# Kernel tuning notes

Hardware: AMD Instinct MI355X
Metric: run time of the kernel (lower is better)

Reference implementation:

```python
import jax, jax.numpy as jnp
import numpy as np

# model dims
B, L, D, K = 4, 1024, 512, 24      # batch, seq_len, d_model, num_eigh
KU, KY, NL, DT = 3, 2, 4, 512      # ar depth u, ar depth y, num_layers, d_target
EPS = 1e-5


def _hankel_eigh():
    # Hankel matrix Z[i,j] = 2 / ((i+j)^3 - (i+j)), i,j in 1..L; top-K eigenpairs
    idx = np.arange(1, L + 1, dtype=np.float64)
    s = idx[:, None] + idx[None, :]
    Z = 2.0 / (s ** 3 - s)
    vals, vecs = np.linalg.eigh(Z)  # ascending
    return (jnp.asarray(vals[-K:], jnp.float32),       # [K]
            jnp.asarray(vecs[:, -K:], jnp.float32))    # [L, K]


def setup_inputs() -> dict:
    key = jax.random.key(0)
    ks = jax.random.split(key, 12)
    sc = 1.0 / np.sqrt(D)
    eig_vals, eig_vecs = _hankel_eigh()
    return {
        "inputs": jax.random.normal(ks[0], (B, L, D), jnp.float32),
        "emb_w": jax.random.normal(ks[1], (D, D), jnp.float32) * sc,
        "emb_b": jnp.zeros((D,), jnp.float32),
        "ln_scale": jnp.ones((NL, D), jnp.float32),
        "ln_bias": jnp.zeros((NL, D), jnp.float32),
        "m_y": jax.random.normal(ks[2], (NL, D, KY, D), jnp.float32) * 0.02,
        "m_u": jax.random.normal(ks[3], (NL, D, D, KU), jnp.float32) * sc,
        "m_phi": jax.random.normal(ks[4], (NL, D * K, D), jnp.float32) * 0.02,
        "w1": jax.random.normal(ks[5], (NL, D, 2 * D), jnp.float32) * sc,
        "b1": jnp.zeros((NL, 2 * D), jnp.float32),
        "proj_w": jax.random.normal(ks[6], (D, DT), jnp.float32) * sc,
        "proj_b": jnp.zeros((DT,), jnp.float32),
        "eig_vals": eig_vals,
        "eig_vecs": eig_vecs,
    }


def _layer_norm(x, s, b):
    mu = jnp.mean(x, axis=-1, keepdims=True)
    var = jnp.mean(jnp.square(x - mu), axis=-1, keepdims=True)
    return (x - mu) * jax.lax.rsqrt(var + EPS) * s + b


def _stu(x, m_y_l, m_u_l, m_phi_l, eig_vals, eig_vecs):
    # x: [B, L, D]
    n = 2 * L
    U = jnp.fft.rfft(x, n=n, axis=1)                 # [B, nf, D]
    V = jnp.fft.rfft(eig_vecs, n=n, axis=0)          # [nf, K]
    # causal conv of each eigvec filter with each channel -> x_tilde [B, L, K, D]
    xt = jnp.fft.irfft(U[:, :, None, :] * V[None, :, :, None], n=n, axis=1)[:, :L]
    xt = xt * (eig_vals[None, None, :, None] ** 0.25)
    delta_phi = xt.reshape(B, L, K * D) @ m_phi_l    # [B, L, D]
    ar = jnp.zeros_like(delta_phi)
    for i in range(KU):
        c = jnp.einsum('bli,oi->blo', x, m_u_l[:, :, i])
        if i > 0:
            c = jnp.pad(c, ((0, 0), (i, 0), (0, 0)))[:, :L]
        ar = ar + c
    deltas = delta_phi + ar
    # y_t = sum_{j<KY} m_y[:,j,:] @ y_{t-1-j} + delta_t  (sequential recurrence)
    def step(carry, d_t):                            # carry [B, KY, D], d_t [B, D]
        y = jnp.einsum('okd,bkd->bo', m_y_l, carry) + d_t
        carry = jnp.concatenate([y[:, None, :], carry[:, :-1]], axis=1)
        return carry, y
    _, ys = jax.lax.scan(step, jnp.zeros((B, KY, D), x.dtype),
                         jnp.transpose(deltas, (1, 0, 2)))
    return jnp.transpose(ys, (1, 0, 2))              # [B, L, D]


def reference(inputs, emb_w, emb_b, ln_scale, ln_bias, m_y, m_u, m_phi,
              w1, b1, proj_w, proj_b, eig_vals, eig_vecs):
    x = inputs @ emb_w + emb_b
    for l in range(NL):
        z = x
        h = _layer_norm(x, ln_scale[l], ln_bias[l])
        h = _stu(h, m_y[l], m_u[l], m_phi[l], eig_vals, eig_vecs)
        h = jax.nn.gelu(h, approximate=False)        # torch GELU default (erf)
        g = h @ w1[l] + b1[l]
        a, b = jnp.split(g, 2, axis=-1)
        h = a * jax.nn.sigmoid(b)                    # GLU(dim=-1)
        x = h + z                                    # residual (dropout=0, eval)
    return x @ proj_w + proj_b
```

## Files before the change

kernel.cpp:

```cpp
#include <hip/hip_runtime.h>
#include <math.h>

typedef __bf16 bf;
typedef __attribute__((ext_vector_type(4))) __bf16 bfv4;
typedef __attribute__((ext_vector_type(8))) __bf16 bfv8;
typedef __attribute__((ext_vector_type(4))) float f32x4;

__device__ __forceinline__ void gload16(const void* g, void* l) {
  __builtin_amdgcn_global_load_lds((const __attribute__((address_space(1))) void*)g,
                                   (__attribute__((address_space(3))) void*)l, 16, 0, 0);
}

struct GOp {
  const bf* A; long la, lKa, lMa, sAz; int zshA, kzA;
  const bf* B; long lb, lKb, sBz; int zmskB, kzB;
  float* C; long ldc, sCz;
  bf* Cb; long ldcb, sCbz;
  const float* bias; int K, maskCmp, mBlk, spS;
};

template<int tB,int tF32,int tB16,int tMASK,int tACC>
__device__ __forceinline__ void gbody(const GOp g, int z, long m0, long n0,
                                      bf* lsA, bf* lsB, const bf* zpg) {
  const int t = threadIdx.x;
  const bf* Ap = g.A + (long)(z >> g.zshA) * g.sAz;
  const bf* Bp = g.B + (long)(z & g.zmskB) * g.sBz;
  const int w = t >> 6, l = t & 63;
  const int wm = (w >> 1) * 64, wn = (w & 1) * 64;
  const int lr = l & 15, lk = (l >> 4) * 8;
  const int r0 = t >> 2, ko = (t & 3) * 8;
  const long rowA1 = m0 + r0, rowA2 = rowA1 + 64;
  const long baseA1 = (rowA1 >> 9) * g.lMa + (rowA1 & 511) * g.la;
  const long baseA2 = (rowA2 >> 9) * g.lMa + (rowA2 & 511) * g.la;
  const long baseB1 = (n0 + r0) * g.lb;
  const int zbA = z * g.kzA, zbB = z * g.kzB;
  const int ct = ((int)rowA1 + 1) & 7;
  const long convB = (long)ct * 2065 + 1023 - (long)rowA1;
  const int Kend = (tMASK == 3) ? ((g.K < (int)m0 + 128) ? g.K : (int)m0 + 128) : g.K;
  f32x4 acc[4][4];
  #pragma unroll
  for (int i = 0; i < 4; i++)
    #pragma unroll
    for (int j = 0; j < 4; j++) acc[i][j] = (f32x4){0.f, 0.f, 0.f, 0.f};

  for (int k0 = 0; k0 < Kend; k0 += 32) {
    const int kk = k0 + ko;
    const int bA = (kk >> 9) + zbA, bB = (kk >> 9) + zbB;
    const long kb = (long)bB * g.lKb + (kk & 511);
    const bf* ga; const bf* ga2;
    if (tMASK == 3) {
      ga  = Ap + convB + kk;
      ga2 = ga - 64;
    } else {
      const long ka = (long)bA * g.lKa + (kk & 511);
      ga  = Ap + baseA1 + ka;
      ga2 = Ap + baseA2 + ka;
      if (tMASK == 1) { if ((int)(rowA1 & 15) < bA) { ga = zpg; ga2 = zpg; } }
      if (tMASK == 2) { if ((int)(rowA1 & 63) < g.maskCmp) { ga = zpg; ga2 = zpg; } }
    }
    const bf* gb = Bp + baseB1 + kb;
    gload16(ga,             &lsA[t * 8]);
    gload16(ga2,            &lsA[2048 + t * 8]);
    gload16(gb,             &lsB[t * 8]);
    gload16(gb + 64 * g.lb, &lsB[2048 + t * 8]);
    __syncthreads();
    bfv8 av[4], bv[4];
    #pragma unroll
    for (int i = 0; i < 4; i++) av[i] = *(const bfv8*)&lsA[(wm + i * 16 + lr) * 32 + lk];
    #pragma unroll
    for (int i = 0; i < 4; i++) bv[i] = *(const bfv8*)&lsB[(wn + i * 16 + lr) * 32 + lk];
    #pragma unroll
    for (int i = 0; i < 4; i++)
      #pragma unroll
      for (int j = 0; j < 4; j++)
        acc[i][j] = __builtin_amdgcn_mfma_f32_16x16x32_bf16(av[i], bv[j], acc[i][j], 0, 0, 0);
    __syncthreads();
  }
  const int orow = (l >> 4) * 4, ocol = lr;
  #pragma unroll
  for (int i = 0; i < 4; i++)
    #pragma unroll
    for (int j = 0; j < 4; j++) {
      long col = n0 + wn + j * 16 + ocol;
      float bb = tB ? g.bias[col] : 0.f;
      #pragma unroll
      for (int r = 0; r < 4; r++) {
        long row = m0 + wm + i * 16 + orow + r;
        float v = acc[i][j][r] + bb;
        if (tF32) {
          long idx = (long)z * g.sCz + row * g.ldc + col;
          if (tACC) v += g.C[idx];
          g.C[idx] = v;
        }
        if (tB16) g.Cb[(long)z * g.sCbz + row * g.ldcb + col] = (bf)v;
      }
    }
}

template<int tB,int tF32,int tB16,int tMASK,int tACC,int tPAIR=0,int tSPEC=0,
         int sB=0,int sF32=0,int sB16=0,int sMASK=0,int sACC=0>
__global__ __launch_bounds__(256) void gemm_k(GOp g, GOp gx, GOp gy, int Zmain,
                                              const bf* __restrict__ zpg) {
  __shared__ bf lsA[4096], lsB[4096];
  int z = blockIdx.z;
  if (tSPEC && z >= Zmain) {
    int flat = (z - Zmain) * (int)(gridDim.x * gridDim.y)
             + (int)blockIdx.y * (int)gridDim.x + (int)blockIdx.x;
    if (flat >= gx.mBlk) return;
    int dxT = gx.spS * 32;
    if (flat < dxT) {
      int zz = flat >> 5, t32 = flat & 31;
      gbody<sB,sF32,sB16,sMASK,sACC>(gx, zz, (long)(t32 >> 3) * 128, (long)(t32 & 7) * 128,
                                     lsA, lsB, zpg);
    } else {
      int f = flat - dxT;
      gbody<sB,sF32,sB16,sMASK,sACC>(gy, 0, (long)(f >> 3) * 128, (long)(f & 7) * 128,
                                     lsA, lsB, zpg);
    }
  } else {
    gbody<tB,tF32,tB16,tMASK,tACC>(g, z, (long)blockIdx.x * 128, (long)blockIdx.y * 128,
                                   lsA, lsB, zpg);
    if (tPAIR)
      gbody<tB,tF32,tB16,tMASK,tACC>(g, z, (long)(2 * gridDim.x - 1 - blockIdx.x) * 128,
                                     (long)blockIdx.y * 128, lsA, lsB, zpg);
  }
}

static inline GOp mkop(const void* A, long la, long lKa, long lMa, long sAz, int zshA, int kzA,
                       const void* B, long lb, long lKb, long sBz, int zmskB, int kzB,
                       void* C, long ldc, long sCz, void* Cb, long ldcb, long sCbz,
                       const void* bias, int K) {
  GOp g;
  g.A = (const bf*)A; g.la = la; g.lKa = lKa; g.lMa = lMa; g.sAz = sAz; g.zshA = zshA; g.kzA = kzA;
  g.B = (const bf*)B; g.lb = lb; g.lKb = lKb; g.sBz = sBz; g.zmskB = zmskB; g.kzB = kzB;
  g.C = (float*)C; g.ldc = ldc; g.sCz = sCz;
  g.Cb = (bf*)Cb; g.ldcb = ldcb; g.sCbz = sCbz;
  g.bias = (const float*)bias; g.K = K; g.maskCmp = 0; g.mBlk = 0; g.spS = 0;
  return g;
}

template<int tB,int tF32,int tB16,int tMASK,int tACC,int tPAIR=0,int tSPEC=0,
         int sB=0,int sF32=0,int sB16=0,int sMASK=0,int sACC=0>
static inline void LG(hipStream_t st, int gx_, int gy_, int gz_, const GOp& g,
                      const GOp& gsx, const GOp& gsy, int Zmain, const bf* zpg) {
  gemm_k<tB,tF32,tB16,tMASK,tACC,tPAIR,tSPEC,sB,sF32,sB16,sMASK,sACC>
      <<<dim3(gx_, gy_, gz_), 256, 0, st>>>(g, gsx, gsy, Zmain, zpg);
}


template<typename TI, typename TO>
__global__ __launch_bounds__(256) void k_trt(const TI* __restrict__ in, TO* __restrict__ out,
                                             long ldin, long inz, long ldout, long outz) {
  __shared__ float tile[64][65];
  int z = blockIdx.z;
  int c0 = blockIdx.x * 64, r0 = blockIdx.y * 64;
  int tx = threadIdx.x & 63, ty = threadIdx.x >> 6;
  #pragma unroll
  for (int i = ty; i < 64; i += 4) tile[i][tx] = (float)in[(long)z * inz + (long)(c0 + i) * ldin + r0 + tx];
  __syncthreads();
  #pragma unroll
  for (int i = ty; i < 64; i += 4) out[(long)z * outz + (long)(r0 + i) * ldout + c0 + tx] = (TO)tile[tx][i];
}

__global__ __launch_bounds__(256) void k_trtS(const float* __restrict__ in, bf* __restrict__ out,
                                              long ldin, long ldout, const float* __restrict__ scl) {
  __shared__ float tile[64][65];
  int c0 = blockIdx.x * 64, r0 = blockIdx.y * 64;
  int tx = threadIdx.x & 63, ty = threadIdx.x >> 6;
  #pragma unroll
  for (int i = ty; i < 64; i += 4) tile[i][tx] = in[(long)(c0 + i) * ldin + r0 + tx];
  __syncthreads();
  float sc = scl[(c0 + tx) >> 9];
  #pragma unroll
  for (int i = ty; i < 64; i += 4) out[(long)(r0 + i) * ldout + c0 + tx] = (bf)(tile[tx][i] * sc);
}

__global__ void k_scl(const float* __restrict__ evals, float* __restrict__ scl) {
  int k = threadIdx.x;
  if (k < 24) scl[k] = powf(evals[k], 0.25f);
}

__global__ void k_pvec(const float* __restrict__ evecs, bf* __restrict__ out) {
  long id = (long)blockIdx.x * 256 + threadIdx.x;
  if (id >= 24L * 16512) return;
  int kf = (int)(id / 16512);
  int rem = (int)(id % 16512);
  int c = rem / 2064, j = rem % 2064;
  int d = j - c;
  float v = (d >= 0 && d <= 1023) ? evecs[(long)(1023 - d) * 24 + kf] : 0.f;
  out[id] = (bf)v;
}

__global__ void k_mut(const float* __restrict__ mul_, bf* __restrict__ out) {
  long id = (long)blockIdx.x * 256 + threadIdx.x;
  long r = id >> 9; int d = (int)(id & 511);
  int i = (int)(r >> 9), o = (int)(r & 511);
  out[id] = (bf)mul_[(long)o * 1536 + d * 3 + i];
}

__global__ __launch_bounds__(256) void k_prep(const float* __restrict__ myl,
                                              bf* __restrict__ ptop, bf* __restrict__ trs) {
  __shared__ float t[64][65];
  long bid = blockIdx.x;
  if (bid < 768) {
    long id = bid * 2048 + (long)threadIdx.x * 8;
    #pragma unroll
    for (int u = 0; u < 8; ++u) {
      long i = id + u;
      if (i < 524288) {
        ptop[15L * 524288 + i] = (bf)myl[i];
      } else if (i < 1048576) {
        long i2 = i - 524288;
        int p = (int)(i2 >> 10), q = (int)(i2 & 1023);
        ptop[16L * 524288 + i2] = (bf)((q == p) ? 1.f : 0.f);
      } else {
        long i3 = i - 1048576;
        int x = (int)(i3 >> 9), y = (int)(i3 & 511);
        trs[(long)x * 1024 + 512 + y] = (bf)((x == y) ? 1.f : 0.f);
      }
    }
  } else {
    int tile = (int)(bid - 768);
    int txx = tile >> 3, tyy = tile & 7;
    int lx = threadIdx.x & 63, ly = threadIdx.x >> 6;
    #pragma unroll
    for (int i = ly; i < 64; i += 4)
      t[i][lx] = myl[(long)(tyy * 64 + i) * 1024 + txx * 64 + lx];
    __syncthreads();
    #pragma unroll
    for (int i = ly; i < 64; i += 4)
      trs[(long)(txx * 64 + i) * 1024 + tyy * 64 + lx] = (bf)t[lx][i];
  }
}

__global__ __launch_bounds__(256) void k_ln(const float* __restrict__ x, const float* __restrict__ sc,
                                            const float* __restrict__ bi, bf* __restrict__ hb) {
  __shared__ float red[8];
  long row = blockIdx.x;
  const float* xr = x + row * 512;
  int t = threadIdx.x;
  float a = xr[t], b2 = xr[t + 256];
  float s = a + b2;
  #pragma unroll
  for (int o = 32; o; o >>= 1) s += __shfl_down(s, o, 64);
  if ((t & 63) == 0) red[t >> 6] = s;
  __syncthreads();
  float mu = (red[0] + red[1] + red[2] + red[3]) * (1.f / 512.f);
  __syncthreads();
  float c1 = a - mu, c2 = b2 - mu;
  float qq = c1 * c1 + c2 * c2;
  #pragma unroll
  for (int o = 32; o; o >>= 1) qq += __shfl_down(qq, o, 64);
  if ((t & 63) == 0) red[t >> 6] = qq;
  __syncthreads();
  float var = (red[0] + red[1] + red[2] + red[3]) * (1.f / 512.f);
  float rs = rsqrtf(var + 1e-5f);
  hb[row * 512 + t]       = (bf)(c1 * rs * sc[t] + bi[t]);
  hb[row * 512 + t + 256] = (bf)(c2 * rs * sc[t + 256] + bi[t + 256]);
}

__global__ void k_deltasS(const float* __restrict__ dp, long stride, int S,
                          const bf* __restrict__ callb, bf* __restrict__ db) {
  long id = (long)blockIdx.x * 256 + threadIdx.x;
  int o = (int)(id & 511); long row = id >> 9; int tt = (int)(row & 1023);
  float v = 0.f;
  for (int zz = 0; zz < S; ++zz) v += dp[(long)zz * stride + id];
  for (int i = 0; i < 3; ++i)
    if (tt >= i) v += (float)callb[(row - i) * 1536 + i * 512 + o];
  db[id] = (bf)v;
}

__global__ void k_egather(const float* __restrict__ dp, long stride, int S,
                          float* __restrict__ E, bf* __restrict__ eb0) {
  long id = (long)blockIdx.x * 256 + threadIdx.x;
  int p = (int)(id & 1023); long r = id >> 10;
  int b = (int)(r >> 6), c = (int)(r & 63);
  int tq = c * 16 + ((p < 512) ? 15 : 14);
  long idx = ((long)(b << 10) + tq) * 512 + (p & 511);
  float v = 0.f;
  for (int zz = 0; zz < S; ++zz) v += dp[(long)zz * stride + idx];
  E[id] = v; eb0[id] = (bf)v;
}

__global__ void k_sfinal(const float* __restrict__ E, bf* __restrict__ ssb) {
  long id = (long)blockIdx.x * 256 + threadIdx.x;
  int c = (int)((id >> 10) & 63);
  ssb[id] = (c > 0) ? (bf)E[id - 1024] : (bf)0.f;
}

__global__ void k_combgelu(const float* __restrict__ dp, long stride, int S,
                           const bf* __restrict__ outh, bf* __restrict__ yg) {
  long id = (long)blockIdx.x * 256 + threadIdx.x;
  int o = (int)(id & 511); long row = id >> 9;
  int b = (int)(row >> 10), tt = (int)(row & 1023);
  int c = tt >> 4, j = tt & 15;
  long wv = ((long)(j * 512 + o)) * 256 + b * 64 + c;
  float v = (float)outh[wv];
  for (int zz = 0; zz < S; ++zz) v += dp[(long)zz * stride + id];
  yg[id] = (bf)(0.5f * v * (1.f + erff(v * 0.70710678118654752f)));
}

__global__ void k_glures(const bf* __restrict__ g, float* __restrict__ x) {
  long id = (long)blockIdx.x * 256 + threadIdx.x;
  int o = (int)(id & 511); long row = id >> 9;
  float a = (float)g[row * 1024 + o], bb = (float)g[row * 1024 + 512 + o];
  x[id] = x[id] + a / (1.f + expf(-bb));
}

__global__ void k_cast(const float* __restrict__ in, bf* __restrict__ out, long n4) {
  long id = (long)blockIdx.x * 256 + threadIdx.x;
  if (id >= n4) return;
  float4 v = *(const float4*)(in + id * 4);
  bfv4 o; o[0] = (bf)v.x; o[1] = (bf)v.y; o[2] = (bf)v.z; o[3] = (bf)v.w;
  *(bfv4*)(out + id * 4) = o;
}

__global__ void k_fill(float* p, long n, float v) {
  long id = (long)blockIdx.x * 256 + threadIdx.x;
  if (id < n) p[id] = v;
}

struct Lay {
  long ZPG, SSTB, SCL, EMBT, PROJT, PVEC, PTOP, TRS, WU, X, MPHITL, MUTL, W1TL,
       HB, HTB, DSLOT, DP, RC, E, EB0, EB1, need;
  int nk, S;
};
static Lay mkLay(int nk, int S) {
  Lay L; long o = 0;
  auto al = [&](long sz) { long r = o; o += (sz + 255) & ~255L; return r; };
  L.nk = nk; L.S = S;
  L.ZPG   = al(4096);
  L.SSTB  = al(524288);
  L.SCL   = al(256);
  L.EMBT  = al(524288);
  L.PROJT = al(524288);
  L.PVEC  = al(24L * 16512 * 2);
  L.PTOP  = al(17L * 1048576);
  L.TRS   = al(2L * 2097152);
  L.WU    = al(8388608);
  L.X     = al(8388608);
  L.MPHITL= al(12582912);
  L.MUTL  = al(1572864);
  L.W1TL  = al(1048576);
  L.HB    = al(4194304);
  L.HTB   = al(4194304);
  L.DSLOT = al(4194304);
  L.DP    = al((long)S * 8388608);
  long rc = (long)nk * 4194304;
  if (rc < 16777216) rc = 16777216;
  L.RC    = al(rc);
  L.E     = al(1048576);
  L.EB0   = al(524288);
  L.EB1   = al(524288);
  L.need  = o;
  return L;
}

extern "C" void kernel_launch(void* const* d_in, const int* in_sizes, int n_in,
                              void* d_out, int out_size, void* d_ws, size_t ws_size,
                              hipStream_t stream) {
  Lay L = mkLay(12, 4);
  if (L.need > (long)ws_size) L = mkLay(8, 4);
  if (L.need > (long)ws_size) L = mkLay(4, 2);
  if (L.need > (long)ws_size) {
    k_fill<<<8192, 256, 0, stream>>>((float*)d_out, 2097152, 1.0e6f + (float)(ws_size >> 20));
    return;
  }
  const float* inp  = (const float*)d_in[0];
  const float* embw = (const float*)d_in[1];
  const float* embb = (const float*)d_in[2];
  const float* lns  = (const float*)d_in[3];
  const float* lnb  = (const float*)d_in[4];
  const float* m_y  = (const float*)d_in[5];
  const float* m_u  = (const float*)d_in[6];
  const float* mphi = (const float*)d_in[7];
  const float* w1   = (const float*)d_in[8];
  const float* b1   = (const float*)d_in[9];
  const float* pw   = (const float*)d_in[10];
  const float* pb   = (const float*)d_in[11];
  const float* evals = (const float*)d_in[12];
  const float* evecs = (const float*)d_in[13];

  char* w = (char*)d_ws;
  bf*    ZPG   = (bf*)(w + L.ZPG);
  bf*    SSTB  = (bf*)(w + L.SSTB);
  float* SCL   = (float*)(w + L.SCL);
  bf*    EMBT  = (bf*)(w + L.EMBT);
  bf*    PROJT = (bf*)(w + L.PROJT);
  bf*    PVEC  = (bf*)(w + L.PVEC);
  bf*    PTOP  = (bf*)(w + L.PTOP);
  bf*    TRSa  = (bf*)(w + L.TRS);
  bf*    TRSb  = TRSa + 1048576;
  bf*    WUa   = (bf*)(w + L.WU);
  bf*    WUb   = (bf*)(w + L.WU + 4194304);
  float* X     = (float*)(w + L.X);
  bf*    MPHITL= (bf*)(w + L.MPHITL);
  bf*    MUTL  = (bf*)(w + L.MUTL);
  bf*    W1TL  = (bf*)(w + L.W1TL);
  bf*    HB    = (bf*)(w + L.HB);
  bf*    HTB   = (bf*)(w + L.HTB);
  bf*    DELTAB= (bf*)(w + L.DSLOT);
  bf*    YGB   = (bf*)(w + L.DSLOT);
  float* DP    = (float*)(w + L.DP);
  bf*    XTC   = (bf*)(w + L.RC);
  bf*    CALLB = (bf*)(w + L.RC);
  bf*    OUTH  = (bf*)(w + L.RC + 12582912);
  bf*    G     = (bf*)(w + L.RC);
  float* E     = (float*)(w + L.E);
  bf*    EB0   = (bf*)(w + L.EB0);
  bf*    EB1   = (bf*)(w + L.EB1);
  bf*    INB   = HB;
  hipStream_t st = stream;
  const int nk = L.nk, S = L.S, nchunk = 24 / nk;
  const long DPS = 2097152;
  const int Kcphi = nk * 512 / S, kzphi = Kcphi >> 9;
  const int Kcy = 8192 / S, kzy = Kcy >> 9;
  GOp gnull = {};
  const int BIGZ = 1 << 30;

  hipMemsetAsync(w + L.ZPG, 0, 4096, st);

  k_scl<<<1, 32, 0, st>>>(evals, SCL);
  k_pvec<<<1549, 256, 0, st>>>(evecs, PVEC);
  k_trt<float, bf><<<dim3(8, 8, 1), 256, 0, st>>>(embw, EMBT, 512, 0, 512, 0);
  k_trt<float, bf><<<dim3(8, 8, 1), 256, 0, st>>>(pw, PROJT, 512, 0, 512, 0);
  k_cast<<<2048, 256, 0, st>>>(inp, INB, 524288);
  LG<1,1,0,0,0>(st, 32, 4, 1,
      mkop(INB, 512, 512, 262144, 0, 30, 0, EMBT, 512, 512, 0, 0, 0,
           X, 512, 0, nullptr, 0, 0, embb, 512), gnull, gnull, BIGZ, ZPG);

  for (int l = 0; l < 4; ++l) {
    k_prep<<<896, 256, 0, st>>>(m_y + (long)l * 524288, PTOP, TRSa);
    k_trtS<<<dim3(192, 8, 1), 256, 0, st>>>(mphi + (long)l * 6291456, MPHITL, 512, 12288, SCL);
    k_mut<<<3072, 256, 0, st>>>(m_u + (long)l * 786432, MUTL);
    k_trt<float, bf><<<dim3(8, 16, 1), 256, 0, st>>>(w1 + (long)l * 524288, W1TL, 1024, 0, 512, 0);

    k_ln<<<4096, 256, 0, st>>>(X, lns + l * 512, lnb + l * 512, HB);
    k_trt<bf, bf><<<dim3(16, 8, 4), 256, 0, st>>>(HB, HTB, 512, 524288, 1024, 524288);

    int hostRound = 0;
    auto mkDXY = [&](int s, bf* TRScur, bf* TRSnxt, GOp& dx, GOp& dy) {
      dx = mkop(PTOP + 15L * 524288, 1024, 512, 0, -524288L, 0, 0,
                TRScur, 1024, 512, 0, 0, 0,
                nullptr, 0, 0, PTOP + (long)(15 - s) * 524288, 1024, -524288L,
                nullptr, 1024);
      dx.mBlk = 32 * s + 64; dx.spS = s;
      dy = mkop(TRScur, 1024, 512, 524288, 0, 0, 0,
                PTOP + (long)(16 - s) * 524288, 1024, 512, 0, 0, 0,
                nullptr, 0, 0, TRSnxt, 1024, 0, nullptr, 1024);
    };
    for (int kc = 0; kc < nchunk; ++kc) {
      GOp gconv = mkop(PVEC + (long)kc * nk * 16512, 0, 0, 0, 16512, 2, 0,
                       HTB, 1024, 512, 524288, 3, 0,
                       nullptr, 0, 0, XTC, 512, 524288, nullptr, 1024);
      if (hostRound < 4) {
        int s = 1 << hostRound;
        bf* TRScur = (hostRound & 1) ? TRSb : TRSa;
        bf* TRSnxt = (hostRound & 1) ? TRSa : TRSb;
        GOp dx, dy; mkDXY(s, TRScur, TRSnxt, dx, dy);
        int nzs = (dx.mBlk + 15) / 16;
        LG<0,0,1,3,0, 1,1, 0,0,1,0,0>(st, 4, 4, 4 * nk + nzs, gconv, dx, dy, 4 * nk, ZPG);
        ++hostRound;
      } else {
        LG<0,0,1,3,0, 1,0>(st, 4, 4, 4 * nk, gconv, gnull, gnull, BIGZ, ZPG);
      }
      GOp gphi = mkop(XTC, 512, 2097152, 262144, 0, 30, kzphi,
                      MPHITL + (long)kc * nk * 512, 12288, 512, 0, 0, kzphi,
                      DP, 512, DPS, nullptr, 0, 0, nullptr, Kcphi);
      if (hostRound < 4) {
        int s = 1 << hostRound;
        bf* TRScur = (hostRound & 1) ? TRSb : TRSa;
        bf* TRSnxt = (hostRound & 1) ? TRSa : TRSb;
        GOp dx, dy; mkDXY(s, TRScur, TRSnxt, dx, dy);
        int nzs = (dx.mBlk + 127) / 128;
        if (kc == 0) LG<0,1,0,0,0, 0,1, 0,0,1,0,0>(st, 32, 4, S + nzs, gphi, dx, dy, S, ZPG);
        else         LG<0,1,0,0,1, 0,1, 0,0,1,0,0>(st, 32, 4, S + nzs, gphi, dx, dy, S, ZPG);
        ++hostRound;
      } else {
        if (kc == 0) LG<0,1,0,0,0>(st, 32, 4, S, gphi, gnull, gnull, BIGZ, ZPG);
        else         LG<0,1,0,0,1>(st, 32, 4, S, gphi, gnull, gnull, BIGZ, ZPG);
      }
    }

    LG<0,0,1,0,0>(st, 32, 12, 1,
        mkop(HB, 512, 512, 262144, 0, 30, 0, MUTL, 512, 512, 0, 0, 0,
             nullptr, 0, 0, CALLB, 1536, 0, nullptr, 512), gnull, gnull, BIGZ, ZPG);
    k_deltasS<<<8192, 256, 0, st>>>(DP, DPS, S, CALLB, DELTAB);

    LG<0,1,0,1,0>(st, 32, 4, S,
        mkop(DELTAB, 512, -512, 262144, 0, 30, kzy,
             PTOP + 16L * 524288, 1024, -524288L, 0, 0, kzy,
             DP, 512, DPS, nullptr, 0, 0, nullptr, Kcy), gnull, gnull, BIGZ, ZPG);

    k_egather<<<1024, 256, 0, st>>>(DP, DPS, S, E, EB0);
    const bf* Wc = PTOP;
    const bf* Uc = TRSa;
    bf* EBc = EB0; bf* EBn = EB1;
    bf* WUn = WUa;
    for (int k = 1; k <= 5; ++k) {
      int sh = 1 << (k - 1);
      GOp mn = mkop(Wc, 1024, 512, 524288, (long)(Uc - Wc), 0, 0,
                    Uc, 1024, 512, (long)(Wc - Uc), 1, 0,
                    nullptr, 0, 0, WUn, 1024, 1048576, nullptr, 1024);
      GOp sp = mkop(EBc - (long)sh * 1024, 1024, 512, 524288, 0, 30, 0,
                    Wc, 1024, 512, 0, 0, 0,
                    E, 1024, 0, EBn, 1024, 0, nullptr, 1024);
      sp.maskCmp = sh; sp.mBlk = 16; sp.spS = 99;
      int gzN = (k < 5) ? 3 : 2, zm = (k < 5) ? 2 : 1;
      LG<0,0,1,0,0, 0,1, 0,1,1,2,1>(st, 8, 8, gzN, mn, sp, gnull, zm, ZPG);
      Wc = WUn; Uc = WUn + 1048576;
      WUn = (k & 1) ? WUb : WUa;
      bf* tmp = EBc; EBc = EBn; EBn = tmp;
    }
    GOp fe = mkop(EBc - 32L * 1024, 1024, 512, 524288, 0, 30, 0,
                  Wc, 1024, 512, 0, 0, 0,
                  E, 1024, 0, nullptr, 0, 0, nullptr, 1024);
    fe.maskCmp = 32;
    LG<0,1,0,2,1>(st, 2, 8, 1, fe, gnull, gnull, BIGZ, ZPG);
    k_sfinal<<<1024, 256, 0, st>>>(E, SSTB);

    LG<0,0,1,0,0>(st, 64, 2, 1,
        mkop(PTOP + 15L * 524288, 1024, 512, -524288L, 0, 30, 0,
             SSTB, 1024, 512, 0, 0, 0,
             nullptr, 0, 0, OUTH, 256, 0, nullptr, 1024), gnull, gnull, BIGZ, ZPG);
    k_combgelu<<<8192, 256, 0, st>>>(DP, DPS, S, OUTH, YGB);
    LG<1,0,1,0,0>(st, 32, 8, 1,
        mkop(YGB, 512, 512, 262144, 0, 30, 0, W1TL, 512, 512, 0, 0, 0,
             nullptr, 0, 0, G, 1024, 0, b1 + (long)l * 1024, 512), gnull, gnull, BIGZ, ZPG);
    k_glures<<<8192, 256, 0, st>>>(G, X);
  }

  k_cast<<<2048, 256, 0, st>>>(X, INB, 524288);
  LG<1,1,0,0,0>(st, 32, 4, 1,
      mkop(INB, 512, 512, 262144, 0, 30, 0, PROJT, 512, 512, 0, 0, 0,
           (float*)d_out, 512, 0, nullptr, 0, 0, pb, 512), gnull, gnull, BIGZ, ZPG);
}
```

Measured before the change: 2.651 ms.

## Overlap scan-doubling matrix products with earlier GEMMs and fuse final shift

Moves the first two matrix-power doubling products (W·U squarings) off the sequential chain by running them as extra blocks inside the m_u GEMM and the local-y GEMM launches. The remaining chain steps are unrolled explicitly with hardcoded buffer ping-pong. The final state GEMM now writes its bf16 output shifted by one row (tSHW), with rows zeroed by memset, which removes the k_sfinal kernel. This targets serial launch latency and idle CUs in the recurrence solve, at the cost of more complex buffer aliasing that must exactly match the old ordering.

```diff
diff --git a/kernel.cpp b/kernel.cpp
--- a/kernel.cpp
+++ b/kernel.cpp
@@ -19,7 +19,7 @@
   const float* bias; int K, maskCmp, mBlk, spS;
 };
 
-template<int tB,int tF32,int tB16,int tMASK,int tACC>
+template<int tB,int tF32,int tB16,int tMASK,int tACC,int tSHW=0>
 __device__ __forceinline__ void gbody(const GOp g, int z, long m0, long n0,
                                       bf* lsA, bf* lsB, const bf* zpg) {
   const int t = threadIdx.x;
@@ -92,13 +92,20 @@
           if (tACC) v += g.C[idx];
           g.C[idx] = v;
         }
-        if (tB16) g.Cb[(long)z * g.sCbz + row * g.ldcb + col] = (bf)v;
+        if (tB16) {
+          if (tSHW) {
+            if ((row & 63) != 63)
+              g.Cb[(long)z * g.sCbz + (row + 1) * g.ldcb + col] = (bf)v;
+          } else {
+            g.Cb[(long)z * g.sCbz + row * g.ldcb + col] = (bf)v;
+          }
+        }
       }
     }
 }
 
 template<int tB,int tF32,int tB16,int tMASK,int tACC,int tPAIR=0,int tSPEC=0,
-         int sB=0,int sF32=0,int sB16=0,int sMASK=0,int sACC=0>
+         int sB=0,int sF32=0,int sB16=0,int sMASK=0,int sACC=0,int tSHW=0>
 __global__ __launch_bounds__(256) void gemm_k(GOp g, GOp gx, GOp gy, int Zmain,
                                               const bf* __restrict__ zpg) {
   __shared__ bf lsA[4096], lsB[4096];
@@ -118,11 +125,11 @@
                                      lsA, lsB, zpg);
     }
   } else {
-    gbody<tB,tF32,tB16,tMASK,tACC>(g, z, (long)blockIdx.x * 128, (long)blockIdx.y * 128,
-                                   lsA, lsB, zpg);
+    gbody<tB,tF32,tB16,tMASK,tACC,tSHW>(g, z, (long)blockIdx.x * 128, (long)blockIdx.y * 128,
+                                        lsA, lsB, zpg);
     if (tPAIR)
-      gbody<tB,tF32,tB16,tMASK,tACC>(g, z, (long)(2 * gridDim.x - 1 - blockIdx.x) * 128,
-                                     (long)blockIdx.y * 128, lsA, lsB, zpg);
+      gbody<tB,tF32,tB16,tMASK,tACC,tSHW>(g, z, (long)(2 * gridDim.x - 1 - blockIdx.x) * 128,
+                                          (long)blockIdx.y * 128, lsA, lsB, zpg);
   }
 }
 
@@ -140,10 +147,10 @@
 }
 
 template<int tB,int tF32,int tB16,int tMASK,int tACC,int tPAIR=0,int tSPEC=0,
-         int sB=0,int sF32=0,int sB16=0,int sMASK=0,int sACC=0>
+         int sB=0,int sF32=0,int sB16=0,int sMASK=0,int sACC=0,int tSHW=0>
 static inline void LG(hipStream_t st, int gx_, int gy_, int gz_, const GOp& g,
                       const GOp& gsx, const GOp& gsy, int Zmain, const bf* zpg) {
-  gemm_k<tB,tF32,tB16,tMASK,tACC,tPAIR,tSPEC,sB,sF32,sB16,sMASK,sACC>
+  gemm_k<tB,tF32,tB16,tMASK,tACC,tPAIR,tSPEC,sB,sF32,sB16,sMASK,sACC,tSHW>
       <<<dim3(gx_, gy_, gz_), 256, 0, st>>>(g, gsx, gsy, Zmain, zpg);
 }
 
@@ -280,12 +287,6 @@
   float v = 0.f;
   for (int zz = 0; zz < S; ++zz) v += dp[(long)zz * stride + idx];
   E[id] = v; eb0[id] = (bf)v;
-}
-
-__global__ void k_sfinal(const float* __restrict__ E, bf* __restrict__ ssb) {
-  long id = (long)blockIdx.x * 256 + threadIdx.x;
-  int c = (int)((id >> 10) & 63);
-  ssb[id] = (c > 0) ? (bf)E[id - 1024] : (bf)0.f;
 }
 
 __global__ void k_combgelu(const float* __restrict__ dp, long stride, int S,
@@ -419,6 +420,8 @@
   const int BIGZ = 1 << 30;
 
   hipMemsetAsync(w + L.ZPG, 0, 4096, st);
+  for (int b = 0; b < 4; ++b)
+    hipMemsetAsync(w + L.SSTB + (long)b * 64 * 2048, 0, 2048, st);
 
   k_scl<<<1, 32, 0, st>>>(evals, SCL);
   k_pvec<<<1549, 256, 0, st>>>(evecs, PVEC);
@@ -482,42 +485,86 @@
       }
     }
 
-    LG<0,0,1,0,0>(st, 32, 12, 1,
-        mkop(HB, 512, 512, 262144, 0, 30, 0, MUTL, 512, 512, 0, 0, 0,
-             nullptr, 0, 0, CALLB, 1536, 0, nullptr, 512), gnull, gnull, BIGZ, ZPG);
+    {
+      GOp gcall = mkop(HB, 512, 512, 262144, 0, 30, 0, MUTL, 512, 512, 0, 0, 0,
+                       nullptr, 0, 0, CALLB, 1536, 0, nullptr, 512);
+      GOp w2x = mkop(PTOP, 1024, 512, 0, 524288, 0, 0,
+                     TRSa, 1024, 512, 0, 0, 0,
+                     nullptr, 0, 0, WUa, 1024, 524288, nullptr, 1024);
+      w2x.mBlk = 128; w2x.spS = 2;
+      GOp u2y = mkop(TRSa, 1024, 512, 524288, 0, 0, 0,
+                     PTOP, 1024, 512, 0, 0, 0,
+                     nullptr, 0, 0, WUa + 1048576, 1024, 0, nullptr, 1024);
+      LG<0,0,1,0,0, 0,1, 0,0,1,0,0>(st, 32, 12, 2, gcall, w2x, u2y, 1, ZPG);
+    }
     k_deltasS<<<8192, 256, 0, st>>>(DP, DPS, S, CALLB, DELTAB);
 
-    LG<0,1,0,1,0>(st, 32, 4, S,
-        mkop(DELTAB, 512, -512, 262144, 0, 30, kzy,
-             PTOP + 16L * 524288, 1024, -524288L, 0, 0, kzy,
-             DP, 512, DPS, nullptr, 0, 0, nullptr, Kcy), gnull, gnull, BIGZ, ZPG);
+    {
+      GOp gyloc = mkop(DELTAB, 512, -512, 262144, 0, 30, kzy,
+                       PTOP + 16L * 524288, 1024, -524288L, 0, 0, kzy,
+                       DP, 512, DPS, nullptr, 0, 0, nullptr, Kcy);
+      GOp w4x = mkop(WUa, 1024, 512, 0, 524288, 0, 0,
+                     WUa + 1048576, 1024, 512, 0, 0, 0,
+                     nullptr, 0, 0, WUb, 1024, 524288, nullptr, 1024);
+      w4x.mBlk = 128; w4x.spS = 2;
+      GOp u4y = mkop(WUa + 1048576, 1024, 512, 524288, 0, 0, 0,
+                     WUa, 1024, 512, 0, 0, 0,
+                     nullptr, 0, 0, WUb + 1048576, 1024, 0, nullptr, 1024);
+      LG<0,1,0,1,0, 0,1, 0,0,1,0,0>(st, 32, 4, S + 1, gyloc, w4x, u4y, S, ZPG);
+    }
 
     k_egather<<<1024, 256, 0, st>>>(DP, DPS, S, E, EB0);
-    const bf* Wc = PTOP;
-    const bf* Uc = TRSa;
-    bf* EBc = EB0; bf* EBn = EB1;
-    bf* WUn = WUa;
-    for (int k = 1; k <= 5; ++k) {
-      int sh = 1 << (k - 1);
-      GOp mn = mkop(Wc, 1024, 512, 524288, (long)(Uc - Wc), 0, 0,
-                    Uc, 1024, 512, (long)(Wc - Uc), 1, 0,
-                    nullptr, 0, 0, WUn, 1024, 1048576, nullptr, 1024);
-      GOp sp = mkop(EBc - (long)sh * 1024, 1024, 512, 524288, 0, 30, 0,
-                    Wc, 1024, 512, 0, 0, 0,
-                    E, 1024, 0, EBn, 1024, 0, nullptr, 1024);
-      sp.maskCmp = sh; sp.mBlk = 16; sp.spS = 99;
-      int gzN = (k < 5) ? 3 : 2, zm = (k < 5) ? 2 : 1;
-      LG<0,0,1,0,0, 0,1, 0,1,1,2,1>(st, 8, 8, gzN, mn, sp, gnull, zm, ZPG);
-      Wc = WUn; Uc = WUn + 1048576;
-      WUn = (k & 1) ? WUb : WUa;
-      bf* tmp = EBc; EBc = EBn; EBn = tmp;
-    }
-    GOp fe = mkop(EBc - 32L * 1024, 1024, 512, 524288, 0, 30, 0,
-                  Wc, 1024, 512, 0, 0, 0,
-                  E, 1024, 0, nullptr, 0, 0, nullptr, 1024);
-    fe.maskCmp = 32;
-    LG<0,1,0,2,1>(st, 2, 8, 1, fe, gnull, gnull, BIGZ, ZPG);
-    k_sfinal<<<1024, 256, 0, st>>>(E, SSTB);
+    {
+      GOp e1 = mkop(EB0 - 1024, 1024, 512, 524288, 0, 30, 0,
+                    PTOP, 1024, 512, 0, 0, 0,
+                    E, 1024, 0, EB1, 1024, 0, nullptr, 1024);
+      e1.maskCmp = 1;
+      LG<0,1,1,2,1>(st, 2, 8, 1, e1, gnull, gnull, BIGZ, ZPG);
+    }
+    {
+      GOp e2 = mkop(EB1 - 2048, 1024, 512, 524288, 0, 30, 0,
+                    WUa, 1024, 512, 0, 0, 0,
+                    E, 1024, 0, EB0, 1024, 0, nullptr, 1024);
+      e2.maskCmp = 2;
+      LG<0,1,1,2,1>(st, 2, 8, 1, e2, gnull, gnull, BIGZ, ZPG);
+    }
+    {
+      GOp mn8 = mkop(WUb, 1024, 512, 524288, 1048576, 0, 0,
+                     WUb + 1048576, 1024, 512, -1048576, 1, 0,
+                     nullptr, 0, 0, WUa, 1024, 1048576, nullptr, 1024);
+      GOp sp3 = mkop(EB0 - 4096, 1024, 512, 524288, 0, 30, 0,
+                     WUb, 1024, 512, 0, 0, 0,
+                     E, 1024, 0, EB1, 1024, 0, nullptr, 1024);
+      sp3.maskCmp = 4; sp3.mBlk = 16; sp3.spS = 99;
+      LG<0,0,1,0,0, 0,1, 0,1,1,2,1>(st, 8, 8, 3, mn8, sp3, gnull, 2, ZPG);
+    }
+    {
+      GOp mn16 = mkop(WUa, 1024, 512, 524288, 1048576, 0, 0,
+                      WUa + 1048576, 1024, 512, -1048576, 1, 0,
+                      nullptr, 0, 0, WUb, 1024, 1048576, nullptr, 1024);
+      GOp sp4 = mkop(EB1 - 8192, 1024, 512, 524288, 0, 30, 0,
+                     WUa, 1024, 512, 0, 0, 0,
+                     E, 1024, 0, EB0, 1024, 0, nullptr, 1024);
+      sp4.maskCmp = 8; sp4.mBlk = 16; sp4.spS = 99;
+      LG<0,0,1,0,0, 0,1, 0,1,1,2,1>(st, 8, 8, 3, mn16, sp4, gnull, 2, ZPG);
+    }
+    {
+      GOp mn32 = mkop(WUb, 1024, 512, 524288, 1048576, 0, 0,
+                      WUb + 1048576, 1024, 512, -1048576, 1, 0,
+                      nullptr, 0, 0, WUa, 1024, 1048576, nullptr, 1024);
+      GOp sp5 = mkop(EB0 - 16384, 1024, 512, 524288, 0, 30, 0,
+                     WUb, 1024, 512, 0, 0, 0,
+                     E, 1024, 0, EB1, 1024, 0, nullptr, 1024);
+      sp5.maskCmp = 16; sp5.mBlk = 16; sp5.spS = 99;
+      LG<0,0,1,0,0, 0,1, 0,1,1,2,1>(st, 8, 8, 2, mn32, sp5, gnull, 1, ZPG);
+    }
+    {
+      GOp fe = mkop(EB1 - 32768, 1024, 512, 524288, 0, 30, 0,
+                    WUa, 1024, 512, 0, 0, 0,
+                    E, 1024, 0, SSTB, 1024, 0, nullptr, 1024);
+      fe.maskCmp = 32;
+      LG<0,1,1,2,1, 0,0, 0,0,0,0,0, 1>(st, 2, 8, 1, fe, gnull, gnull, BIGZ, ZPG);
+    }
 
     LG<0,0,1,0,0>(st, 64, 2, 1,
         mkop(PTOP + 15L * 524288, 1024, 512, -524288L, 0, 30, 0,
```

After: 2.687 ms. Within noise of the previous version (+1.4%).
